# Optimization experiments

Measured on AMD Instinct MI355X. Metric: run time of the kernel, lower is better.

Reference implementation:

```python
import jax, jax.numpy as jnp
import numpy as np

WINDOW_SIZE = 11
SIGMA = 1.5
CHANNELS = 3
DATA_RANGE = 1.0


def _create_window(window_size, channel):
    x = np.arange(window_size) - window_size // 2
    g = np.exp(-(x ** 2) / (2.0 * SIGMA ** 2))
    g = g / g.sum()
    w2d = np.outer(g, g).astype(np.float32)  # [ws, ws]
    # depthwise kernel, OIHW with I=1, O=channel
    return jnp.asarray(np.broadcast_to(w2d, (channel, 1, window_size, window_size)).copy())


def _depthwise_conv(x, window, channel):
    # x: [B, C, H, W], window: [C, 1, ws, ws], VALID padding, groups=C
    return jax.lax.conv_general_dilated(
        x, window, window_strides=(1, 1), padding='VALID',
        dimension_numbers=('NCHW', 'OIHW', 'NCHW'),
        feature_group_count=channel)


def setup_inputs() -> dict:
    key = jax.random.key(0)
    k1, k2 = jax.random.split(key)
    img1 = jax.random.uniform(k1, (32, CHANNELS, 512, 512), dtype=jnp.float32)
    img2 = jax.random.uniform(k2, (32, CHANNELS, 512, 512), dtype=jnp.float32)
    return {"img1": img1, "img2": img2}


def reference(img1, img2):
    channel = img1.shape[1]
    window = _create_window(WINDOW_SIZE, channel).astype(img1.dtype)

    mu1 = _depthwise_conv(img1, window, channel)
    mu2 = _depthwise_conv(img2, window, channel)
    mu1_sq = mu1 * mu1
    mu2_sq = mu2 * mu2
    mu1_mu2 = mu1 * mu2

    sigma1_sq = _depthwise_conv(img1 * img1, window, channel) - mu1_sq
    sigma2_sq = _depthwise_conv(img2 * img2, window, channel) - mu2_sq
    sigma12 = _depthwise_conv(img1 * img2, window, channel) - mu1_mu2

    C1 = (0.01 * DATA_RANGE) ** 2
    C2 = (0.03 * DATA_RANGE) ** 2
    v1 = 2.0 * sigma12 + C2
    v2 = sigma1_sq + sigma2_sq + C2
    ssim_map = (2.0 * mu1_mu2 + C1) * v1 / ((mu1_sq + mu2_sq + C1) * v2)
    # mean over channel, height, width -> per-image SSIM [B]
    return ssim_map.mean(axis=(1, 2, 3))
```

## Files before the change

### kernel.cpp

```cpp
#include <hip/hip_runtime.h>

#define H 512
#define W 512
#define OUT_Wc 502
#define OUT_Hc 502
#define C1c 1.0e-4f
#define C2c 9.0e-4f

#define TH 56
#define NR 66
#define RW 266
#define HALO 10

__global__ __launch_bounds__(256, 4) void ssim_kernel(const float* __restrict__ img1,
                                                      const float* __restrict__ img2,
                                                      float* __restrict__ out) {
    __shared__ float2 ring[4][RW];

    constexpr float GW[11] = {0.00102838f, 0.00759876f, 0.03600078f, 0.10936067f,
                              0.21300555f, 0.26601174f, 0.21300555f, 0.10936067f,
                              0.03600078f, 0.00759876f, 0.00102838f};

    const int tid = threadIdx.x;
    const int X0 = blockIdx.x * 256;
    const int Y0 = blockIdx.y * TH;
    const int plane = blockIdx.z;
    const size_t pbase = (size_t)plane * (H * W);
    const float* __restrict__ p1 = img1 + pbase;
    const float* __restrict__ p2 = img2 + pbase;

    const int gx = X0 + tid;
    const int hx = min(X0 + 256 + tid, W - 1);

    float as_[11], ad_[11], aq_[11], ar_[11];
#pragma unroll
    for (int i = 0; i < 11; ++i) { as_[i]=0.f; ad_[i]=0.f; aq_[i]=0.f; ar_[i]=0.f; }

    const bool colok = (gx < OUT_Wc);
    float lsum = 0.f;

    float n0a, n0b, n1a, n1b, h0a, h0b, h1a, h1b;
    float m0a, m0b, m1a, m1b, k0a, k0b, k1a, k1b;
    {
        const float* r0a = p1 + (size_t)Y0 * W;
        const float* r0b = p2 + (size_t)Y0 * W;
        const float* r1a = r0a + W;
        const float* r1b = r0b + W;
        float x0a = r0a[gx], x0b = r0b[gx], x1a = r1a[gx], x1b = r1b[gx];
        ring[0][tid] = make_float2(x0a + x0b, x0a - x0b);
        ring[1][tid] = make_float2(x1a + x1b, x1a - x1b);
        if (tid < HALO) {
            float y0a = r0a[hx], y0b = r0b[hx], y1a = r1a[hx], y1b = r1b[hx];
            ring[0][256 + tid] = make_float2(y0a + y0b, y0a - y0b);
            ring[1][256 + tid] = make_float2(y1a + y1b, y1a - y1b);
        }
        const float* r2a = r0a + 2 * W;  const float* r2b = r0b + 2 * W;
        const float* r3a = r0a + 3 * W;  const float* r3b = r0b + 3 * W;
        const float* r4a = r0a + 4 * W;  const float* r4b = r0b + 4 * W;
        const float* r5a = r0a + 5 * W;  const float* r5b = r0b + 5 * W;
        n0a = r2a[gx]; n0b = r2b[gx]; n1a = r3a[gx]; n1b = r3b[gx];
        m0a = r4a[gx]; m0b = r4b[gx]; m1a = r5a[gx]; m1b = r5b[gx];
        h0a=h0b=h1a=h1b=k0a=k0b=k1a=k1b=0.f;
        if (tid < HALO) {
            h0a = r2a[hx]; h0b = r2b[hx]; h1a = r3a[hx]; h1b = r3b[hx];
            k0a = r4a[hx]; k0b = r4b[hx]; k1a = r5a[hx]; k1b = r5b[hx];
        }
    }
    __syncthreads();

#define ROW_STEP(SLOT, PH, RRT)                                               \
    {                                                                         \
        const float2* __restrict__ rp = &ring[(SLOT)][tid];                   \
        float hs, hd, hq, hr;                                                 \
        _Pragma("unroll")                                                     \
        for (int t = 0; t < 11; ++t) {                                        \
            const float2 v = rp[t];                                           \
            const float w = GW[t];                                            \
            if (t == 0) { hs = w*v.x; hd = w*v.y;                             \
                          hq = w*(v.x*v.x); hr = w*(v.y*v.y); }               \
            else { hs = fmaf(w, v.x, hs); hd = fmaf(w, v.y, hd);              \
                   hq = fmaf(w, v.x*v.x, hq); hr = fmaf(w, v.y*v.y, hr); }    \
        }                                                                     \
        _Pragma("unroll")                                                     \
        for (int a = 0; a < 11; ++a) {                                        \
            const float w = GW[((PH) - a + 11) % 11];                         \
            if (a == (PH)) { as_[a]=w*hs; ad_[a]=w*hd; aq_[a]=w*hq; ar_[a]=w*hr; } \
            else { as_[a]=fmaf(w,hs,as_[a]); ad_[a]=fmaf(w,hd,ad_[a]);        \
                   aq_[a]=fmaf(w,hq,aq_[a]); ar_[a]=fmaf(w,hr,ar_[a]); }      \
        }                                                                     \
        const int e = ((PH) + 1) % 11;                                        \
        const int oy = Y0 + (RRT) - 10;                                       \
        if ((RRT) >= 10 && oy < OUT_Hc) {                                     \
            const float ms = as_[e], md = ad_[e], qs = aq_[e], qd = ar_[e];   \
            const float A = ms * ms, B = md * md;                             \
            const float u = A - B, vv = A + B;                                \
            const float w2 = qs - qd, z = qs + qd;                            \
            const float num_a = fmaf(0.5f, u, C1c);                           \
            const float den_a = fmaf(0.5f, vv, C1c);                          \
            const float num_b = fmaf(0.5f, w2 - u, C2c);                      \
            const float den_b = fmaf(0.5f, z - vv, C2c);                      \
            const float val = (num_a * num_b) * __builtin_amdgcn_rcpf(den_a * den_b); \
            lsum += colok ? val : 0.f;                                        \
        }                                                                     \
    }

#pragma unroll 1
    for (int rb = 0; rb < NR; rb += 22) {
#pragma unroll
        for (int pp = 0; pp < 11; ++pp) {
            const int p = 2 * pp;
            const int r = rb + p;

            const int gy6 = min(Y0 + r + 6, H - 1);
            const int gy7 = min(Y0 + r + 7, H - 1);
            const float* __restrict__ A6 = p1 + (size_t)gy6 * W;
            const float* __restrict__ B6 = p2 + (size_t)gy6 * W;
            const float* __restrict__ A7 = p1 + (size_t)gy7 * W;
            const float* __restrict__ B7 = p2 + (size_t)gy7 * W;
            const float t0a = A6[gx], t0b = B6[gx], t1a = A7[gx], t1b = B7[gx];
            float u0a = 0.f, u0b = 0.f, u1a = 0.f, u1b = 0.f;
            if (tid < HALO) { u0a = A6[hx]; u0b = B6[hx]; u1a = A7[hx]; u1b = B7[hx]; }

            const int s2 = (r + 2) & 3, s3 = (r + 3) & 3;
            ring[s2][tid] = make_float2(n0a + n0b, n0a - n0b);
            ring[s3][tid] = make_float2(n1a + n1b, n1a - n1b);
            if (tid < HALO) {
                ring[s2][256 + tid] = make_float2(h0a + h0b, h0a - h0b);
                ring[s3][256 + tid] = make_float2(h1a + h1b, h1a - h1b);
            }
            n0a = m0a; n0b = m0b; n1a = m1a; n1b = m1b;
            h0a = k0a; h0b = k0b; h1a = k1a; h1b = k1b;
            m0a = t0a; m0b = t0b; m1a = t1a; m1b = t1b;
            k0a = u0a; k0b = u0b; k1a = u1a; k1b = u1b;

            ROW_STEP((r) & 3,     (2 * pp) % 11,     r);
            ROW_STEP((r + 1) & 3, (2 * pp + 1) % 11, r + 1);

            __syncthreads();
        }
    }
#undef ROW_STEP

#pragma unroll
    for (int off = 32; off > 0; off >>= 1) lsum += __shfl_down(lsum, off, 64);
    if ((tid & 63) == 0) {
        const float inv_count = 1.0f / (3.0f * (float)OUT_Hc * (float)OUT_Wc);
        atomicAdd(&out[plane / 3], lsum * inv_count);
    }
}

__global__ void zero_out(float* out, int n) {
    int i = threadIdx.x + blockIdx.x * blockDim.x;
    if (i < n) out[i] = 0.f;
}

extern "C" void kernel_launch(void* const* d_in, const int* in_sizes, int n_in,
                              void* d_out, int out_size, void* d_ws, size_t ws_size,
                              hipStream_t stream) {
    const float* img1 = (const float*)d_in[0];
    const float* img2 = (const float*)d_in[1];
    float* out = (float*)d_out;

    zero_out<<<1, 64, 0, stream>>>(out, out_size);

    const int nplanes = in_sizes[0] / (H * W);
    dim3 grid(2,
              (OUT_Hc + TH - 1) / TH,
              nplanes);
    ssim_kernel<<<grid, 256, 0, stream>>>(img1, img2, out);
}
```

Before: 271.3 us.

## Give each wavefront a private LDS ring and replace block barriers with wave barriers

Each 64-lane wavefront now owns its own 64-column strip, with a private shared-memory ring buffer holding 64+10 columns. This lets the per-row __syncthreads be replaced by wave-level barriers, so waves no longer stall on each other. The cost is more halo work, since each wave loads a 10-column halo instead of each block loading one. The launch-bounds occupancy hint also drops from 4 to 3. The kernel relies on the lockstep execution of a wavefront for correctness of the shared-memory writes and reads.

```diff
diff --git a/kernel.cpp b/kernel.cpp
--- a/kernel.cpp
+++ b/kernel.cpp
@@ -9,28 +9,32 @@
 
 #define TH 56
 #define NR 66
-#define RW 266
-#define HALO 10
+#define RSTRIDE 80
 
-__global__ __launch_bounds__(256, 4) void ssim_kernel(const float* __restrict__ img1,
+__global__ __launch_bounds__(256, 3) void ssim_kernel(const float* __restrict__ img1,
                                                       const float* __restrict__ img2,
                                                       float* __restrict__ out) {
-    __shared__ float2 ring[4][RW];
+    __shared__ float2 ring[4][4][RSTRIDE];
 
     constexpr float GW[11] = {0.00102838f, 0.00759876f, 0.03600078f, 0.10936067f,
                               0.21300555f, 0.26601174f, 0.21300555f, 0.10936067f,
                               0.03600078f, 0.00759876f, 0.00102838f};
 
-    const int tid = threadIdx.x;
-    const int X0 = blockIdx.x * 256;
-    const int Y0 = blockIdx.y * TH;
+    const int tid  = threadIdx.x;
+    const int wv   = tid >> 6;
+    const int lane = tid & 63;
+
     const int plane = blockIdx.z;
     const size_t pbase = (size_t)plane * (H * W);
     const float* __restrict__ p1 = img1 + pbase;
     const float* __restrict__ p2 = img2 + pbase;
 
-    const int gx = X0 + tid;
-    const int hx = min(X0 + 256 + tid, W - 1);
+    const int Y0    = blockIdx.y * TH;
+    const int wcol0 = (blockIdx.x * 4 + wv) * 64;
+    const int gx    = wcol0 + lane;
+    const int hx    = min(wcol0 + 64 + lane, W - 1);
+
+    float2 (* __restrict__ wring)[RSTRIDE] = ring[wv];
 
     float as_[11], ad_[11], aq_[11], ar_[11];
 #pragma unroll
@@ -47,12 +51,12 @@
         const float* r1a = r0a + W;
         const float* r1b = r0b + W;
         float x0a = r0a[gx], x0b = r0b[gx], x1a = r1a[gx], x1b = r1b[gx];
-        ring[0][tid] = make_float2(x0a + x0b, x0a - x0b);
-        ring[1][tid] = make_float2(x1a + x1b, x1a - x1b);
-        if (tid < HALO) {
+        wring[0][lane] = make_float2(x0a + x0b, x0a - x0b);
+        wring[1][lane] = make_float2(x1a + x1b, x1a - x1b);
+        if (lane < 10) {
             float y0a = r0a[hx], y0b = r0b[hx], y1a = r1a[hx], y1b = r1b[hx];
-            ring[0][256 + tid] = make_float2(y0a + y0b, y0a - y0b);
-            ring[1][256 + tid] = make_float2(y1a + y1b, y1a - y1b);
+            wring[0][64 + lane] = make_float2(y0a + y0b, y0a - y0b);
+            wring[1][64 + lane] = make_float2(y1a + y1b, y1a - y1b);
         }
         const float* r2a = r0a + 2 * W;  const float* r2b = r0b + 2 * W;
         const float* r3a = r0a + 3 * W;  const float* r3b = r0b + 3 * W;
@@ -61,16 +65,16 @@
         n0a = r2a[gx]; n0b = r2b[gx]; n1a = r3a[gx]; n1b = r3b[gx];
         m0a = r4a[gx]; m0b = r4b[gx]; m1a = r5a[gx]; m1b = r5b[gx];
         h0a=h0b=h1a=h1b=k0a=k0b=k1a=k1b=0.f;
-        if (tid < HALO) {
+        if (lane < 10) {
             h0a = r2a[hx]; h0b = r2b[hx]; h1a = r3a[hx]; h1b = r3b[hx];
             k0a = r4a[hx]; k0b = r4b[hx]; k1a = r5a[hx]; k1b = r5b[hx];
         }
     }
-    __syncthreads();
+    __builtin_amdgcn_wave_barrier();
 
 #define ROW_STEP(SLOT, PH, RRT)                                               \
     {                                                                         \
-        const float2* __restrict__ rp = &ring[(SLOT)][tid];                   \
+        const float2* __restrict__ rp = &wring[(SLOT)][lane];                 \
         float hs, hd, hq, hr;                                                 \
         _Pragma("unroll")                                                     \
         for (int t = 0; t < 11; ++t) {                                        \
@@ -108,8 +112,7 @@
     for (int rb = 0; rb < NR; rb += 22) {
 #pragma unroll
         for (int pp = 0; pp < 11; ++pp) {
-            const int p = 2 * pp;
-            const int r = rb + p;
+            const int r = rb + 2 * pp;
 
             const int gy6 = min(Y0 + r + 6, H - 1);
             const int gy7 = min(Y0 + r + 7, H - 1);
@@ -119,31 +122,33 @@
             const float* __restrict__ B7 = p2 + (size_t)gy7 * W;
             const float t0a = A6[gx], t0b = B6[gx], t1a = A7[gx], t1b = B7[gx];
             float u0a = 0.f, u0b = 0.f, u1a = 0.f, u1b = 0.f;
-            if (tid < HALO) { u0a = A6[hx]; u0b = B6[hx]; u1a = A7[hx]; u1b = B7[hx]; }
+            if (lane < 10) { u0a = A6[hx]; u0b = B6[hx]; u1a = A7[hx]; u1b = B7[hx]; }
 
             const int s2 = (r + 2) & 3, s3 = (r + 3) & 3;
-            ring[s2][tid] = make_float2(n0a + n0b, n0a - n0b);
-            ring[s3][tid] = make_float2(n1a + n1b, n1a - n1b);
-            if (tid < HALO) {
-                ring[s2][256 + tid] = make_float2(h0a + h0b, h0a - h0b);
-                ring[s3][256 + tid] = make_float2(h1a + h1b, h1a - h1b);
+            wring[s2][lane] = make_float2(n0a + n0b, n0a - n0b);
+            wring[s3][lane] = make_float2(n1a + n1b, n1a - n1b);
+            if (lane < 10) {
+                wring[s2][64 + lane] = make_float2(h0a + h0b, h0a - h0b);
+                wring[s3][64 + lane] = make_float2(h1a + h1b, h1a - h1b);
             }
             n0a = m0a; n0b = m0b; n1a = m1a; n1b = m1b;
             h0a = k0a; h0b = k0b; h1a = k1a; h1b = k1b;
             m0a = t0a; m0b = t0b; m1a = t1a; m1b = t1b;
             k0a = u0a; k0b = u0b; k1a = u1a; k1b = u1b;
 
+            __builtin_amdgcn_wave_barrier();
+
             ROW_STEP((r) & 3,     (2 * pp) % 11,     r);
             ROW_STEP((r + 1) & 3, (2 * pp + 1) % 11, r + 1);
 
-            __syncthreads();
+            __builtin_amdgcn_wave_barrier();
         }
     }
 #undef ROW_STEP
 
 #pragma unroll
     for (int off = 32; off > 0; off >>= 1) lsum += __shfl_down(lsum, off, 64);
-    if ((tid & 63) == 0) {
+    if (lane == 0) {
         const float inv_count = 1.0f / (3.0f * (float)OUT_Hc * (float)OUT_Wc);
         atomicAdd(&out[plane / 3], lsum * inv_count);
     }
```

After: 275.3 us. About the same (+1.5%).
